# Kernel optimization log

Hardware: AMD Instinct MI355X
Metric: run time of the kernel (lower is better)

## Reference

```python
import jax, jax.numpy as jnp
import numpy as np


def setup_inputs() -> dict:
    key = jax.random.key(0)
    k1, k2 = jax.random.split(key)
    x = jax.random.normal(k1, (4, 64, 32, 64, 64), dtype=jnp.float32)
    # Conv3d(2, 1, kernel_size=7, padding=3, bias=False) weight: [out_c=1, in_c=2, 7, 7, 7]
    conv_w = jax.random.normal(k2, (1, 2, 7, 7, 7), dtype=jnp.float32) * 0.05
    return {"x": x, "conv_w": conv_w}


def reference(x, conv_w):
    # x: [B, C, D, H, W]
    avg_out = jnp.mean(x, axis=1, keepdims=True)          # [B,1,D,H,W]
    max_out = jnp.max(x, axis=1, keepdims=True)           # [B,1,D,H,W]
    pooled = jnp.concatenate([avg_out, max_out], axis=1)  # [B,2,D,H,W]
    att = jax.lax.conv_general_dilated(
        pooled, conv_w,
        window_strides=(1, 1, 1),
        padding=[(3, 3), (3, 3), (3, 3)],
        dimension_numbers=("NCDHW", "OIDHW", "NCDHW"),
    )  # [B,1,D,H,W]
    att = jax.nn.sigmoid(att)
    return x * att
```

## Files before the change

### kernel.cpp

```cpp
#include <hip/hip_runtime.h>
#include <math.h>

#define BB 4
#define CC 64
#define DD 32
#define HH 64
#define WW 64
#define DHW (DD * HH * WW)
#define NP  (BB * DHW)
#define CDHW (CC * DHW)

__global__ void pool_kernel(const float* __restrict__ x,
                            float* __restrict__ out) {
    int tid4 = blockIdx.x * blockDim.x + threadIdx.x;
    int i = tid4 * 4;
    int b = i >> 17;
    int s = i & (DHW - 1);
    const float* base = x + (size_t)b * CDHW + s;
    float4 v = *(const float4*)base;
    float4 sum = v, mx = v;
#pragma unroll 8
    for (int c = 1; c < CC; ++c) {
        float4 u = *(const float4*)(base + (size_t)c * DHW);
        sum.x += u.x; sum.y += u.y; sum.z += u.z; sum.w += u.w;
        mx.x = fmaxf(mx.x, u.x); mx.y = fmaxf(mx.y, u.y);
        mx.z = fmaxf(mx.z, u.z); mx.w = fmaxf(mx.w, u.w);
    }
    const float inv = 1.0f / (float)CC;
    float4 av; av.x = sum.x * inv; av.y = sum.y * inv;
    av.z = sum.z * inv; av.w = sum.w * inv;
    *(float4*)(out + (size_t)b * CDHW + 1 * DHW + s) = av;
    *(float4*)(out + (size_t)b * CDHW + 2 * DHW + s) = mx;
}

#define ROWF 76
#define PLANEF (10 * ROWF)

__global__ __launch_bounds__(256) void conv_kernel(const float* __restrict__ cw,
                                                   float* __restrict__ out) {
    __shared__ float lds[4 * 2 * PLANEF];

    int bx = blockIdx.x;
    int hblk = bx & 3;
    int d = (bx >> 2) & 31;
    int b = bx >> 7;
    int tid = threadIdx.x;
    int wv = tid >> 6, lane = tid & 63;
    int wg = lane & 15, hl = lane >> 4;
    int h0w = (hblk << 4) + (wv << 2);
    int h = h0w + hl;
    int w0 = wg << 2;

    float* region = lds + wv * (2 * PLANEF);

    int roff[3], goff[3]; bool okhc[3]; bool act[3];
#pragma unroll
    for (int j = 0; j < 3; ++j) {
        int k = lane + 64 * j;
        int r = k / 18, c = k - r * 18;
        int hh = h0w - 3 + r;
        act[j]  = (k < 180);
        okhc[j] = act[j] && (hh >= 0) && (hh < HH) && (c >= 1) && (c <= 16);
        roff[j] = r * ROWF + (c << 2);
        goff[j] = (hh << 6) + (c << 2) - 4;
    }

    const float* outb = out + (size_t)b * CDHW;
    float acc0 = 0.f, acc1 = 0.f, acc2 = 0.f, acc3 = 0.f;

    auto load_plane = [&](int p, float4* st) {
        int ch = (p >= 7) ? 1 : 0;
        int kd = p - ch * 7;
        int dd = d + kd - 3;
        bool dok = (dd >= 0) && (dd < DD);
        const float* pb = outb + (size_t)(ch + 1) * DHW + ((size_t)dd << 12);
#pragma unroll
        for (int j = 0; j < 3; ++j) {
            float4 v = make_float4(0.f, 0.f, 0.f, 0.f);
            if (dok && okhc[j]) v = *(const float4*)(pb + goff[j]);
            st[j] = v;
        }
    };
    auto write_plane = [&](float* buf, const float4* st) {
#pragma unroll
        for (int j = 0; j < 3; ++j)
            if (act[j]) *(float4*)(buf + roff[j]) = st[j];
    };
    auto compute_plane = [&](const float* buf, int p) {
        int ch = (p >= 7) ? 1 : 0;
        int kd = p - ch * 7;
        const float* wp = cw + ch * 343 + kd * 49;
#pragma unroll
        for (int kh = 0; kh < 7; ++kh) {
            const float* rp = buf + (hl + kh) * ROWF + w0;
            float4 q0 = *(const float4*)(rp);
            float4 q1 = *(const float4*)(rp + 4);
            float4 q2 = *(const float4*)(rp + 8);
            float a[12] = {q0.x, q0.y, q0.z, q0.w,
                           q1.x, q1.y, q1.z, q1.w,
                           q2.x, q2.y, q2.z, q2.w};
            const float* wr = wp + kh * 7;
#pragma unroll
            for (int kw = 0; kw < 7; ++kw) {
                float wvv = wr[kw];
                acc0 = fmaf(a[kw + 1], wvv, acc0);
                acc1 = fmaf(a[kw + 2], wvv, acc1);
                acc2 = fmaf(a[kw + 3], wvv, acc2);
                acc3 = fmaf(a[kw + 4], wvv, acc3);
            }
        }
    };

    float4 st[3];
    load_plane(0, st);
    write_plane(region, st);
    for (int p = 0; p < 14; ++p) {
        float* cur = region + (p & 1) * PLANEF;
        float* nxt = region + ((p + 1) & 1) * PLANEF;
        float4 nx[3];
        if (p < 13) load_plane(p + 1, nx);
        compute_plane(cur, p);
        if (p < 13) write_plane(nxt, nx);
    }

    size_t o = (size_t)b * CDHW + (size_t)((d << 6) + h) * WW + w0;
    float4 r;
    r.x = 1.f / (1.f + __expf(-acc0));
    r.y = 1.f / (1.f + __expf(-acc1));
    r.z = 1.f / (1.f + __expf(-acc2));
    r.w = 1.f / (1.f + __expf(-acc3));
    *(float4*)(out + o) = r;
}

__global__ void scale_kernel(const float* __restrict__ x,
                             float* __restrict__ out) {
    int tid4 = blockIdx.x * blockDim.x + threadIdx.x;
    int i = tid4 * 4;
    int b = i >> 17;
    int s = i & (DHW - 1);
    size_t base = (size_t)b * CDHW + s;
    float4 av = *(const float4*)(out + base);
#pragma unroll 4
    for (int c = 0; c < CC; ++c) {
        float4 xv = *(const float4*)(x + base + (size_t)c * DHW);
        float4 o;
        o.x = xv.x * av.x; o.y = xv.y * av.y;
        o.z = xv.z * av.z; o.w = xv.w * av.w;
        *(float4*)(out + base + (size_t)c * DHW) = o;
    }
}

extern "C" void kernel_launch(void* const* d_in, const int* in_sizes, int n_in,
                              void* d_out, int out_size, void* d_ws, size_t ws_size,
                              hipStream_t stream) {
    const float* x  = (const float*)d_in[0];
    const float* cw = (const float*)d_in[1];
    float* out = (float*)d_out;

    pool_kernel<<<NP / 4 / 256, 256, 0, stream>>>(x, out);
    conv_kernel<<<BB * DD * (HH / 16), 256, 0, stream>>>(cw, out);
    scale_kernel<<<NP / 4 / 256, 256, 0, stream>>>(x, out);
}
```

Baseline: 291.7 us.

## Fuse conv-sigmoid with channel scaling using workspace for pooled maps

Pooled avg/max maps are written to the workspace, and the conv+sigmoid kernel then directly scales all 64 channels of x. This removes the separate scale kernel and the attention-map round trip through global memory. The cost is that the big streaming pass now runs on only 512 blocks behind the conv compute, which may reduce memory-level parallelism. A fallback keeps the old three-kernel path when the workspace is too small.

```diff
diff --git a/kernel.cpp b/kernel.cpp
--- a/kernel.cpp
+++ b/kernel.cpp
@@ -10,8 +10,13 @@
 #define NP  (BB * DHW)
 #define CDHW (CC * DHW)
 
+#define ROWF 76
+#define PLANEF (10 * ROWF)
+
 __global__ void pool_kernel(const float* __restrict__ x,
-                            float* __restrict__ out) {
+                            float* __restrict__ avgp,
+                            float* __restrict__ maxp,
+                            size_t bstride) {
     int tid4 = blockIdx.x * blockDim.x + threadIdx.x;
     int i = tid4 * 4;
     int b = i >> 17;
@@ -29,29 +34,18 @@
     const float inv = 1.0f / (float)CC;
     float4 av; av.x = sum.x * inv; av.y = sum.y * inv;
     av.z = sum.z * inv; av.w = sum.w * inv;
-    *(float4*)(out + (size_t)b * CDHW + 1 * DHW + s) = av;
-    *(float4*)(out + (size_t)b * CDHW + 2 * DHW + s) = mx;
-}
-
-#define ROWF 76
-#define PLANEF (10 * ROWF)
-
-__global__ __launch_bounds__(256) void conv_kernel(const float* __restrict__ cw,
-                                                   float* __restrict__ out) {
-    __shared__ float lds[4 * 2 * PLANEF];
-
-    int bx = blockIdx.x;
-    int hblk = bx & 3;
-    int d = (bx >> 2) & 31;
-    int b = bx >> 7;
-    int tid = threadIdx.x;
-    int wv = tid >> 6, lane = tid & 63;
+    *(float4*)(avgp + (size_t)b * bstride + s) = av;
+    *(float4*)(maxp + (size_t)b * bstride + s) = mx;
+}
+
+__device__ __forceinline__ float4 conv_sigmoid(const float* __restrict__ avgp,
+                                               const float* __restrict__ maxp,
+                                               size_t bstride,
+                                               const float* __restrict__ cw,
+                                               float* region,
+                                               int b, int d, int h0w, int lane) {
     int wg = lane & 15, hl = lane >> 4;
-    int h0w = (hblk << 4) + (wv << 2);
-    int h = h0w + hl;
     int w0 = wg << 2;
-
-    float* region = lds + wv * (2 * PLANEF);
 
     int roff[3], goff[3]; bool okhc[3]; bool act[3];
 #pragma unroll
@@ -65,7 +59,6 @@
         goff[j] = (hh << 6) + (c << 2) - 4;
     }
 
-    const float* outb = out + (size_t)b * CDHW;
     float acc0 = 0.f, acc1 = 0.f, acc2 = 0.f, acc3 = 0.f;
 
     auto load_plane = [&](int p, float4* st) {
@@ -73,7 +66,8 @@
         int kd = p - ch * 7;
         int dd = d + kd - 3;
         bool dok = (dd >= 0) && (dd < DD);
-        const float* pb = outb + (size_t)(ch + 1) * DHW + ((size_t)dd << 12);
+        const float* pb = (ch == 0 ? avgp : maxp) + (size_t)b * bstride
+                        + ((size_t)dd << 12);
 #pragma unroll
         for (int j = 0; j < 3; ++j) {
             float4 v = make_float4(0.f, 0.f, 0.f, 0.f);
@@ -123,13 +117,63 @@
         if (p < 13) write_plane(nxt, nx);
     }
 
-    size_t o = (size_t)b * CDHW + (size_t)((d << 6) + h) * WW + w0;
     float4 r;
     r.x = 1.f / (1.f + __expf(-acc0));
     r.y = 1.f / (1.f + __expf(-acc1));
     r.z = 1.f / (1.f + __expf(-acc2));
     r.w = 1.f / (1.f + __expf(-acc3));
-    *(float4*)(out + o) = r;
+    return r;
+}
+
+__global__ __launch_bounds__(256) void conv_scale_kernel(
+        const float* __restrict__ x,
+        const float* __restrict__ avgp,
+        const float* __restrict__ maxp,
+        const float* __restrict__ cw,
+        float* __restrict__ out) {
+    __shared__ float lds[4 * 2 * PLANEF];
+    int bx = blockIdx.x;
+    int hblk = bx & 3;
+    int d = (bx >> 2) & 31;
+    int b = bx >> 7;
+    int tid = threadIdx.x;
+    int wv = tid >> 6, lane = tid & 63;
+    int h0w = (hblk << 4) + (wv << 2);
+
+    float4 att = conv_sigmoid(avgp, maxp, DHW, cw,
+                              lds + wv * (2 * PLANEF), b, d, h0w, lane);
+
+    int hl = lane >> 4, w0 = (lane & 15) << 2;
+    int h = h0w + hl;
+    size_t base = (size_t)b * CDHW + (size_t)((d << 6) + h) * WW + w0;
+#pragma unroll 8
+    for (int c = 0; c < CC; ++c) {
+        float4 xv = *(const float4*)(x + base + (size_t)c * DHW);
+        float4 o;
+        o.x = xv.x * att.x; o.y = xv.y * att.y;
+        o.z = xv.z * att.z; o.w = xv.w * att.w;
+        *(float4*)(out + base + (size_t)c * DHW) = o;
+    }
+}
+
+__global__ __launch_bounds__(256) void conv_kernel(const float* __restrict__ cw,
+                                                   float* __restrict__ out) {
+    __shared__ float lds[4 * 2 * PLANEF];
+    int bx = blockIdx.x;
+    int hblk = bx & 3;
+    int d = (bx >> 2) & 31;
+    int b = bx >> 7;
+    int tid = threadIdx.x;
+    int wv = tid >> 6, lane = tid & 63;
+    int h0w = (hblk << 4) + (wv << 2);
+
+    float4 att = conv_sigmoid(out + DHW, out + 2 * DHW, CDHW, cw,
+                              lds + wv * (2 * PLANEF), b, d, h0w, lane);
+
+    int hl = lane >> 4, w0 = (lane & 15) << 2;
+    int h = h0w + hl;
+    size_t o = (size_t)b * CDHW + (size_t)((d << 6) + h) * WW + w0;
+    *(float4*)(out + o) = att;
 }
 
 __global__ void scale_kernel(const float* __restrict__ x,
@@ -140,7 +184,7 @@
     int s = i & (DHW - 1);
     size_t base = (size_t)b * CDHW + s;
     float4 av = *(const float4*)(out + base);
-#pragma unroll 4
+#pragma unroll 8
     for (int c = 0; c < CC; ++c) {
         float4 xv = *(const float4*)(x + base + (size_t)c * DHW);
         float4 o;
@@ -157,7 +201,16 @@
     const float* cw = (const float*)d_in[1];
     float* out = (float*)d_out;
 
-    pool_kernel<<<NP / 4 / 256, 256, 0, stream>>>(x, out);
-    conv_kernel<<<BB * DD * (HH / 16), 256, 0, stream>>>(cw, out);
-    scale_kernel<<<NP / 4 / 256, 256, 0, stream>>>(x, out);
-}
+    if (ws_size >= (size_t)2 * NP * sizeof(float)) {
+        float* avgp = (float*)d_ws;
+        float* maxp = avgp + NP;
+        pool_kernel<<<NP / 4 / 256, 256, 0, stream>>>(x, avgp, maxp, DHW);
+        conv_scale_kernel<<<BB * DD * (HH / 16), 256, 0, stream>>>(
+            x, avgp, maxp, cw, out);
+    } else {
+        pool_kernel<<<NP / 4 / 256, 256, 0, stream>>>(x, out + DHW,
+                                                      out + 2 * DHW, CDHW);
+        conv_kernel<<<BB * DD * (HH / 16), 256, 0, stream>>>(cw, out);
+        scale_kernel<<<NP / 4 / 256, 256, 0, stream>>>(x, out);
+    }
+}
```

Result: faster. 276.7 us (-5.2%).
